# Kernel tuning notes

Measured on AMD Instinct MI355X. Metric: run time of the kernel, lower is better.

The kernel has to match this reference:

```python
import jax, jax.numpy as jnp
import numpy as np

N_FEATURES = 1024
N_HEADS = 16
D_ATTN = 64


def setup_inputs() -> dict:
    key = jax.random.key(0)
    k_x, k_qkv, k_pw, k_pb = jax.random.split(key, 4)
    B, S = 2, 2048
    x = jax.random.normal(k_x, (B, S, N_FEATURES), dtype=jnp.float32)
    # torch nn.Linear weights are [out, in]; init scale ~ 1/sqrt(in)
    w_qkv = jax.random.normal(k_qkv, (3 * N_HEADS * D_ATTN, N_FEATURES), dtype=jnp.float32) / np.sqrt(N_FEATURES)
    w_proj = jax.random.normal(k_pw, (N_FEATURES, N_HEADS * D_ATTN), dtype=jnp.float32) / np.sqrt(N_HEADS * D_ATTN)
    b_proj = jax.random.normal(k_pb, (N_FEATURES,), dtype=jnp.float32) / np.sqrt(N_HEADS * D_ATTN)
    return {"x": x, "w_qkv": w_qkv, "w_proj": w_proj, "b_proj": b_proj}


def reference(x, w_qkv, w_proj, b_proj):
    B, S, F = x.shape
    H, D = N_HEADS, D_ATTN
    # fused QKV projection (bias=False): [B,S,3*H*D]
    qkv = jnp.einsum('bsf,of->bso', x, w_qkv)
    qkv = qkv.reshape(B, S, 3, H, D)
    q = jnp.transpose(qkv[:, :, 0], (0, 2, 1, 3))  # [B,H,S,D]
    k = jnp.transpose(qkv[:, :, 1], (0, 2, 1, 3))
    v = jnp.transpose(qkv[:, :, 2], (0, 2, 1, 3))
    scale = 1.0 / jnp.sqrt(jnp.asarray(D, dtype=x.dtype))
    scores = jnp.einsum('bhqd,bhkd->bhqk', q, k) * scale  # [B,H,S,S]
    attn = jax.nn.softmax(scores, axis=-1)
    out = jnp.einsum('bhqk,bhkd->bhqd', attn, v)  # [B,H,S,D]
    out = jnp.transpose(out, (0, 2, 1, 3)).reshape(B, S, H * D)
    # output projection (dropout is identity in eval mode)
    return jnp.einsum('bsm,fm->bsf', out, w_proj) + b_proj
```

## Files before the change

kernel.cpp:

```cpp
#include <hip/hip_runtime.h>
#include <hip/hip_bf16.h>
#include <math.h>

#define BATCH 2
#define SEQ 2048
#define NFEAT 1024
#define NHEAD 16
#define DHEAD 64
#define MROWS (BATCH * SEQ)
#define NQKV (3 * NHEAD * DHEAD)

typedef __attribute__((ext_vector_type(8))) short short8;
typedef __attribute__((ext_vector_type(4))) float floatx4;

#define CEXP 0.18033688f

__device__ __forceinline__ unsigned short f2bf(float f) {
    unsigned int u = __float_as_uint(f);
    u += 0x7fff + ((u >> 16) & 1);
    return (unsigned short)(u >> 16);
}

__device__ __forceinline__ float fast_exp2(float x) {
    return __builtin_amdgcn_exp2f(x);
}

__device__ __forceinline__ uint pack_bf16x2(float lo, float hi) {
    float2 t; t.x = lo; t.y = hi;
    __hip_bfloat162 h = __float22bfloat162_rn(t);
    union { __hip_bfloat162 h; uint u; } c; c.h = h;
    return c.u;
}

__device__ __forceinline__ void async16(const void* g, void* l) {
    __builtin_amdgcn_global_load_lds(
        (const __attribute__((address_space(1))) void*)g,
        (__attribute__((address_space(3))) void*)l, 16, 0, 0);
}

__global__ void cvt_swz(const float* __restrict__ x, const float* __restrict__ wq,
                        const float* __restrict__ wp,
                        ushort* __restrict__ xb, ushort* __restrict__ wqb,
                        ushort* __restrict__ wpb) {
    const int NX = MROWS * NFEAT / 4, NWQ = NQKV * NFEAT / 4, NWP = NFEAT * NFEAT / 4;
    int i = blockIdx.x * blockDim.x + threadIdx.x;
    if (i >= NX + NWQ + NWP) return;
    const float* src; ushort* dst; int idx4;
    if (i < NX)            { src = x;  dst = xb;  idx4 = i; }
    else if (i < NX + NWQ) { src = wq; dst = wqb; idx4 = i - NX; }
    else                   { src = wp; dst = wpb; idx4 = i - NX - NWQ; }
    float4 v = ((const float4*)src)[idx4];
    ushort4 o;
    o.x = f2bf(v.x); o.y = f2bf(v.y); o.z = f2bf(v.z); o.w = f2bf(v.w);
    const int e = idx4 * 4;
    const int k = e & (NFEAT - 1);
    const int row = e >> 10;
    const int kp = (k & ~31) | (((((k >> 3) & 3) ^ ((row >> 1) & 3))) << 3) | (k & 7);
    *(ushort4*)(dst + (size_t)row * NFEAT + kp) = o;
}

template <int EPI>
__global__ __launch_bounds__(256, 2)
void gemm_bt(const ushort* __restrict__ A, const ushort* __restrict__ W,
             int M, int N, int K,
             ushort* __restrict__ qb, ushort* __restrict__ kb, ushort* __restrict__ vtb,
             const float* __restrict__ bias, float* __restrict__ Cout) {
    __shared__ ushort smem[8192];
    ushort* As = smem;
    ushort* Bs = smem + 4096;
    const int tid = threadIdx.x;
    const int wave = tid >> 6, lane = tid & 63;
    const int m0 = blockIdx.y * 128, n0 = blockIdx.x * 128;
    const int wm = (wave >> 1) * 64, wn = (wave & 1) * 64;
    const int lr = lane & 15, lg = lane >> 4;
    const int kswz = (lg ^ ((lr >> 1) & 3)) * 8;

    floatx4 acc[4][4] = {};

    const int seg0 = tid, seg1 = tid + 256;
    const int row0 = seg0 >> 2, cb0 = (seg0 & 3) * 8;
    const int row1 = seg1 >> 2, cb1 = (seg1 & 3) * 8;

    for (int k0 = 0; k0 < K; k0 += 32) {
        async16(A + (size_t)(m0 + row0) * K + k0 + cb0, (void*)(As + seg0 * 8));
        async16(A + (size_t)(m0 + row1) * K + k0 + cb1, (void*)(As + seg1 * 8));
        async16(W + (size_t)(n0 + row0) * K + k0 + cb0, (void*)(Bs + seg0 * 8));
        async16(W + (size_t)(n0 + row1) * K + k0 + cb1, (void*)(Bs + seg1 * 8));
        __syncthreads();
        short8 a[4], b[4];
#pragma unroll
        for (int i = 0; i < 4; ++i)
            a[i] = *(const short8*)(As + (wm + i * 16 + lr) * 32 + kswz);
#pragma unroll
        for (int j = 0; j < 4; ++j)
            b[j] = *(const short8*)(Bs + (wn + j * 16 + lr) * 32 + kswz);
#pragma unroll
        for (int i = 0; i < 4; ++i)
#pragma unroll
            for (int j = 0; j < 4; ++j)
                acc[i][j] = __builtin_amdgcn_mfma_f32_16x16x32_bf16(a[i], b[j], acc[i][j], 0, 0, 0);
        __syncthreads();
    }

    if (EPI == 1) {
#pragma unroll
        for (int i = 0; i < 4; ++i)
#pragma unroll
            for (int j = 0; j < 4; ++j)
#pragma unroll
                for (int r = 0; r < 4; ++r) {
                    const int m = m0 + wm + i * 16 + lg * 4 + r;
                    const int n = n0 + wn + j * 16 + lr;
                    Cout[(size_t)m * N + n] = acc[i][j][r] + bias[n];
                }
        return;
    }

    const int t = n0 >> 10;
    const int bidx = m0 >> 11;
    if (t < 2) {
#pragma unroll
        for (int i = 0; i < 4; ++i)
#pragma unroll
            for (int j = 0; j < 4; ++j)
#pragma unroll
                for (int r = 0; r < 4; ++r) {
                    const int m = m0 + wm + i * 16 + lg * 4 + r;
                    const int n = n0 + wn + j * 16 + lr;
                    const int s = m & (SEQ - 1);
                    const int rem = n & 1023, h = rem >> 6, d = rem & 63;
                    if (t == 0) {
                        qb[((size_t)(bidx * NHEAD + h) * SEQ + s) * DHEAD + d] =
                            f2bf(acc[i][j][r] * CEXP);
                    } else {
                        const int dcol = ((((d >> 3) ^ (s & 7)) << 3)) | (d & 7);
                        kb[((size_t)(bidx * NHEAD + h) * SEQ + s) * DHEAD + dcol] =
                            f2bf(acc[i][j][r]);
                    }
                }
    } else {
#pragma unroll
        for (int hhalf = 0; hhalf < 2; ++hhalf) {
            if ((wm >> 6) == hhalf) {
#pragma unroll
                for (int i = 0; i < 4; ++i) {
                    const int chunk = i * 2 + (lg >> 1);
#pragma unroll
                    for (int j = 0; j < 4; ++j) {
                        const int n = wn + j * 16 + lr;
                        uint2 pk;
                        pk.x = pack_bf16x2(acc[i][j][0], acc[i][j][1]);
                        pk.y = pack_bf16x2(acc[i][j][2], acc[i][j][3]);
                        *(uint2*)(smem + n * 64 + ((chunk ^ (n & 7)) * 8) + (lg & 1) * 4) = pk;
                    }
                }
            }
            __syncthreads();
            const int s_base = (m0 & (SEQ - 1)) + hhalf * 64;
#pragma unroll
            for (int it = 0; it < 4; ++it) {
                const int n_r = (tid >> 3) + it * 32;
                const int p = tid & 7;
                short8 rowv = *(const short8*)(smem + n_r * 64 + p * 8);
                const int nglob = n0 + n_r;
                const int d = nglob & 63, hh = (nglob & 1023) >> 6;
                *(short8*)(vtb + ((size_t)(bidx * NHEAD + hh) * DHEAD + d) * SEQ + s_base + p * 8) = rowv;
            }
            __syncthreads();
        }
    }
}

__global__ __launch_bounds__(256, 4)
void flash_attn(const ushort* __restrict__ qb, const ushort* __restrict__ kb,
                const ushort* __restrict__ vtb, ushort* __restrict__ aob) {
    const int qt = blockIdx.x, bh = blockIdx.y;
    const int tid = threadIdx.x, wave = tid >> 6, lane = tid & 63;
    const int lr = lane & 15, lg = lane >> 4;

    __shared__ ushort Ks[2][64 * 64];
    __shared__ ushort Vs[2][64 * 64];
    __shared__ ushort Ps_all[4][16 * 64];
    ushort* Ps = Ps_all[wave];

    const ushort* Qb = qb + (size_t)bh * SEQ * DHEAD;
    const ushort* Kb = kb + (size_t)bh * SEQ * DHEAD;
    const ushort* Vt = vtb + (size_t)bh * DHEAD * SEQ;

    const int q0 = qt * 64 + wave * 16;

    short8 qf[2];
#pragma unroll
    for (int kk = 0; kk < 2; ++kk)
        qf[kk] = *(const short8*)(Qb + (size_t)(q0 + lr) * DHEAD + kk * 32 + lg * 8);

    const int kofs = tid * 8;
    const size_t vrow = (size_t)(tid >> 3) * SEQ;
    const int vcol = (tid & 7) * 8;

    async16(Kb + kofs,                    (void*)(Ks[0] + kofs));
    async16(Kb + 2048 + kofs,             (void*)(Ks[0] + 2048 + kofs));
    async16(Vt + vrow + vcol,             (void*)(Vs[0] + kofs));
    async16(Vt + 32 * SEQ + vrow + vcol,  (void*)(Vs[0] + 2048 + kofs));

    floatx4 acc_o[4] = {};
    float l_lane = 0.0f;
    const int sw = lr & 7;

#define FLASH_PREFETCH(BUF, KV)                                                     \
    {                                                                               \
        const int kv_ = (KV);                                                       \
        async16(Kb + (size_t)kv_ * DHEAD + kofs,          (void*)(Ks[BUF] + kofs)); \
        async16(Kb + (size_t)kv_ * DHEAD + 2048 + kofs,   (void*)(Ks[BUF] + 2048 + kofs)); \
        async16(Vt + vrow + kv_ + vcol,                   (void*)(Vs[BUF] + kofs)); \
        async16(Vt + 32 * SEQ + vrow + kv_ + vcol,        (void*)(Vs[BUF] + 2048 + kofs)); \
    }

#define FLASH_COMPUTE(BUF)                                                          \
    {                                                                               \
        floatx4 st[4] = {};                                                         \
        _Pragma("unroll")                                                           \
        for (int kk = 0; kk < 2; ++kk)                                              \
            _Pragma("unroll")                                                       \
            for (int i = 0; i < 4; ++i) {                                           \
                short8 kf = *(const short8*)(Ks[BUF] + (i * 16 + lr) * 64 +         \
                                             (((kk * 4 + lg) ^ sw) * 8));           \
                st[i] = __builtin_amdgcn_mfma_f32_16x16x32_bf16(kf, qf[kk], st[i], 0, 0, 0); \
            }                                                                       \
        _Pragma("unroll")                                                           \
        for (int i = 0; i < 4; ++i) {                                               \
            const float p0 = fast_exp2(st[i][0]);                                   \
            const float p1 = fast_exp2(st[i][1]);                                   \
            const float p2 = fast_exp2(st[i][2]);                                   \
            const float p3 = fast_exp2(st[i][3]);                                   \
            l_lane += (p0 + p1) + (p2 + p3);                                        \
            uint2 pk;                                                               \
            pk.x = pack_bf16x2(p0, p1);                                             \
            pk.y = pack_bf16x2(p2, p3);                                             \
            const int chunk = i * 2 + (lg >> 1);                                    \
            *(uint2*)(Ps + lr * 64 + ((chunk ^ sw) * 8) + (lg & 1) * 4) = pk;       \
        }                                                                           \
        _Pragma("unroll")                                                           \
        for (int kk2 = 0; kk2 < 2; ++kk2) {                                         \
            short8 pf = *(const short8*)(Ps + lr * 64 + (((kk2 * 4 + lg) ^ sw) * 8)); \
            _Pragma("unroll")                                                       \
            for (int j2 = 0; j2 < 4; ++j2) {                                        \
                short8 vf = *(const short8*)(Vs[BUF] + (j2 * 16 + lr) * 64 +        \
                                             (((kk2 * 4 + lg) ^ sw) * 8));          \
                acc_o[j2] = __builtin_amdgcn_mfma_f32_16x16x32_bf16(pf, vf, acc_o[j2], 0, 0, 0); \
            }                                                                       \
        }                                                                           \
    }

    for (int kt = 0; kt < SEQ / 64; kt += 2) {
        __syncthreads();
        FLASH_PREFETCH(1, (kt + 1) * 64)
        FLASH_COMPUTE(0)
        __syncthreads();
        if (kt + 2 < SEQ / 64)
            FLASH_PREFETCH(0, (kt + 2) * 64)
        FLASH_COMPUTE(1)
    }
#undef FLASH_PREFETCH
#undef FLASH_COMPUTE

    l_lane += __shfl_xor(l_lane, 16);
    l_lane += __shfl_xor(l_lane, 32);

    const int b = bh >> 4, h = bh & 15;
#pragma unroll
    for (int r = 0; r < 4; ++r) {
        const float lq = __shfl(l_lane, lg * 4 + r);
        const float invl = 1.0f / lq;
        const int srow = b * SEQ + q0 + lg * 4 + r;
        const int key = (srow >> 1) & 3;
#pragma unroll
        for (int j2 = 0; j2 < 4; ++j2) {
            const int d = j2 * 16 + lr;
            const int dsw = (d & ~31) | (((((d >> 3) & 3) ^ key)) << 3) | (d & 7);
            aob[(size_t)srow * (NHEAD * DHEAD) + h * DHEAD + dsw] = f2bf(acc_o[j2][r] * invl);
        }
    }
}

extern "C" void kernel_launch(void* const* d_in, const int* in_sizes, int n_in,
                              void* d_out, int out_size, void* d_ws, size_t ws_size,
                              hipStream_t stream) {
    const float* x      = (const float*)d_in[0];
    const float* w_qkv  = (const float*)d_in[1];
    const float* w_proj = (const float*)d_in[2];
    const float* b_proj = (const float*)d_in[3];
    float* out = (float*)d_out;

    ushort* ws = (ushort*)d_ws;
    ushort* xb     = ws;
    ushort* wqkvb  = xb + (size_t)MROWS * NFEAT;
    ushort* wprojb = wqkvb + (size_t)NQKV * NFEAT;
    ushort* qb     = wprojb + (size_t)NFEAT * NFEAT;
    ushort* kb     = qb + (size_t)MROWS * NFEAT;
    ushort* vtb    = kb + (size_t)MROWS * NFEAT;
    ushort* aob    = vtb + (size_t)MROWS * NFEAT;

    {
        const int total = (MROWS * NFEAT + NQKV * NFEAT + NFEAT * NFEAT) / 4;
        cvt_swz<<<(total + 255) / 256, 256, 0, stream>>>(x, w_qkv, w_proj, xb, wqkvb, wprojb);
    }

    {
        dim3 grid(NQKV / 128, MROWS / 128);
        gemm_bt<0><<<grid, 256, 0, stream>>>(xb, wqkvb, MROWS, NQKV, NFEAT,
                                             qb, kb, vtb, nullptr, nullptr);
    }

    {
        dim3 grid(SEQ / 64, BATCH * NHEAD);
        flash_attn<<<grid, 256, 0, stream>>>(qb, kb, vtb, aob);
    }

    {
        dim3 grid(NFEAT / 128, MROWS / 128);
        gemm_bt<1><<<grid, 256, 0, stream>>>(aob, wprojb, MROWS, NFEAT, NFEAT,
                                             nullptr, nullptr, nullptr, b_proj, out);
    }
}
```

Before: 194.2 us.

## Process 32 query rows per wave in flash attention and narrow projection GEMM tiles

Flash attention now gives each wave two 16-row query tiles (128 queries per block), so every K and V fragment read from shared memory feeds twice as many MFMAs. This halves the K/V global traffic per query and amortizes the per-tile shared-memory loads. The cost is more registers and doubled P scratch in LDS, so occupancy is lowered to 2 blocks per CU. The output projection moves to a dedicated kernel with 128x64 tiles, doubling its grid from 256 to 512 blocks to fill more CUs.

```diff
diff --git a/kernel.cpp b/kernel.cpp
--- a/kernel.cpp
+++ b/kernel.cpp
@@ -59,12 +59,9 @@
     *(ushort4*)(dst + (size_t)row * NFEAT + kp) = o;
 }
 
-template <int EPI>
 __global__ __launch_bounds__(256, 2)
-void gemm_bt(const ushort* __restrict__ A, const ushort* __restrict__ W,
-             int M, int N, int K,
-             ushort* __restrict__ qb, ushort* __restrict__ kb, ushort* __restrict__ vtb,
-             const float* __restrict__ bias, float* __restrict__ Cout) {
+void gemm_qkv(const ushort* __restrict__ A, const ushort* __restrict__ W,
+              ushort* __restrict__ qb, ushort* __restrict__ kb, ushort* __restrict__ vtb) {
     __shared__ ushort smem[8192];
     ushort* As = smem;
     ushort* Bs = smem + 4096;
@@ -81,11 +78,11 @@
     const int row0 = seg0 >> 2, cb0 = (seg0 & 3) * 8;
     const int row1 = seg1 >> 2, cb1 = (seg1 & 3) * 8;
 
-    for (int k0 = 0; k0 < K; k0 += 32) {
-        async16(A + (size_t)(m0 + row0) * K + k0 + cb0, (void*)(As + seg0 * 8));
-        async16(A + (size_t)(m0 + row1) * K + k0 + cb1, (void*)(As + seg1 * 8));
-        async16(W + (size_t)(n0 + row0) * K + k0 + cb0, (void*)(Bs + seg0 * 8));
-        async16(W + (size_t)(n0 + row1) * K + k0 + cb1, (void*)(Bs + seg1 * 8));
+    for (int k0 = 0; k0 < NFEAT; k0 += 32) {
+        async16(A + (size_t)(m0 + row0) * NFEAT + k0 + cb0, (void*)(As + seg0 * 8));
+        async16(A + (size_t)(m0 + row1) * NFEAT + k0 + cb1, (void*)(As + seg1 * 8));
+        async16(W + (size_t)(n0 + row0) * NFEAT + k0 + cb0, (void*)(Bs + seg0 * 8));
+        async16(W + (size_t)(n0 + row1) * NFEAT + k0 + cb1, (void*)(Bs + seg1 * 8));
         __syncthreads();
         short8 a[4], b[4];
 #pragma unroll
@@ -100,20 +97,6 @@
             for (int j = 0; j < 4; ++j)
                 acc[i][j] = __builtin_amdgcn_mfma_f32_16x16x32_bf16(a[i], b[j], acc[i][j], 0, 0, 0);
         __syncthreads();
-    }
-
-    if (EPI == 1) {
-#pragma unroll
-        for (int i = 0; i < 4; ++i)
-#pragma unroll
-            for (int j = 0; j < 4; ++j)
-#pragma unroll
-                for (int r = 0; r < 4; ++r) {
-                    const int m = m0 + wm + i * 16 + lg * 4 + r;
-                    const int n = n0 + wn + j * 16 + lr;
-                    Cout[(size_t)m * N + n] = acc[i][j][r] + bias[n];
-                }
-        return;
     }
 
     const int t = n0 >> 10;
@@ -171,7 +154,55 @@
     }
 }
 
-__global__ __launch_bounds__(256, 4)
+__global__ __launch_bounds__(256, 2)
+void gemm_proj(const ushort* __restrict__ A, const ushort* __restrict__ W,
+               const float* __restrict__ bias, float* __restrict__ Cout) {
+    __shared__ ushort As[128 * 32];
+    __shared__ ushort Bs[64 * 32];
+    const int tid = threadIdx.x;
+    const int wave = tid >> 6, lane = tid & 63;
+    const int m0 = blockIdx.y * 128, n0 = blockIdx.x * 64;
+    const int wm = (wave >> 1) * 64, wn = (wave & 1) * 32;
+    const int lr = lane & 15, lg = lane >> 4;
+    const int kswz = (lg ^ ((lr >> 1) & 3)) * 8;
+
+    floatx4 acc[4][2] = {};
+
+    const int rowA = tid >> 2, cb = (tid & 3) * 8;
+
+    for (int k0 = 0; k0 < NFEAT; k0 += 32) {
+        async16(A + (size_t)(m0 + rowA) * NFEAT + k0 + cb, (void*)(As + tid * 8));
+        async16(A + (size_t)(m0 + rowA + 64) * NFEAT + k0 + cb, (void*)(As + (tid + 256) * 8));
+        async16(W + (size_t)(n0 + rowA) * NFEAT + k0 + cb, (void*)(Bs + tid * 8));
+        __syncthreads();
+        short8 a[4], b[2];
+#pragma unroll
+        for (int i = 0; i < 4; ++i)
+            a[i] = *(const short8*)(As + (wm + i * 16 + lr) * 32 + kswz);
+#pragma unroll
+        for (int j = 0; j < 2; ++j)
+            b[j] = *(const short8*)(Bs + (wn + j * 16 + lr) * 32 + kswz);
+#pragma unroll
+        for (int i = 0; i < 4; ++i)
+#pragma unroll
+            for (int j = 0; j < 2; ++j)
+                acc[i][j] = __builtin_amdgcn_mfma_f32_16x16x32_bf16(a[i], b[j], acc[i][j], 0, 0, 0);
+        __syncthreads();
+    }
+
+#pragma unroll
+    for (int i = 0; i < 4; ++i)
+#pragma unroll
+        for (int j = 0; j < 2; ++j)
+#pragma unroll
+            for (int r = 0; r < 4; ++r) {
+                const int m = m0 + wm + i * 16 + lg * 4 + r;
+                const int n = n0 + wn + j * 16 + lr;
+                Cout[(size_t)m * NFEAT + n] = acc[i][j][r] + bias[n];
+            }
+}
+
+__global__ __launch_bounds__(256, 2)
 void flash_attn(const ushort* __restrict__ qb, const ushort* __restrict__ kb,
                 const ushort* __restrict__ vtb, ushort* __restrict__ aob) {
     const int qt = blockIdx.x, bh = blockIdx.y;
@@ -180,19 +211,21 @@
 
     __shared__ ushort Ks[2][64 * 64];
     __shared__ ushort Vs[2][64 * 64];
-    __shared__ ushort Ps_all[4][16 * 64];
+    __shared__ ushort Ps_all[4][32 * 64];
     ushort* Ps = Ps_all[wave];
 
     const ushort* Qb = qb + (size_t)bh * SEQ * DHEAD;
     const ushort* Kb = kb + (size_t)bh * SEQ * DHEAD;
     const ushort* Vt = vtb + (size_t)bh * DHEAD * SEQ;
 
-    const int q0 = qt * 64 + wave * 16;
-
-    short8 qf[2];
-#pragma unroll
-    for (int kk = 0; kk < 2; ++kk)
-        qf[kk] = *(const short8*)(Qb + (size_t)(q0 + lr) * DHEAD + kk * 32 + lg * 8);
+    const int q0 = qt * 128 + wave * 32;
+
+    short8 qf[2][2];
+#pragma unroll
+    for (int j = 0; j < 2; ++j)
+#pragma unroll
+        for (int kk = 0; kk < 2; ++kk)
+            qf[j][kk] = *(const short8*)(Qb + (size_t)(q0 + j * 16 + lr) * DHEAD + kk * 32 + lg * 8);
 
     const int kofs = tid * 8;
     const size_t vrow = (size_t)(tid >> 3) * SEQ;
@@ -203,8 +236,8 @@
     async16(Vt + vrow + vcol,             (void*)(Vs[0] + kofs));
     async16(Vt + 32 * SEQ + vrow + vcol,  (void*)(Vs[0] + 2048 + kofs));
 
-    floatx4 acc_o[4] = {};
-    float l_lane = 0.0f;
+    floatx4 acc_o[2][4] = {};
+    float l_lane[2] = {0.0f, 0.0f};
     const int sw = lr & 7;
 
 #define FLASH_PREFETCH(BUF, KV)                                                     \
@@ -218,36 +251,46 @@
 
 #define FLASH_COMPUTE(BUF)                                                          \
     {                                                                               \
-        floatx4 st[4] = {};                                                         \
+        floatx4 st[4][2] = {};                                                      \
         _Pragma("unroll")                                                           \
         for (int kk = 0; kk < 2; ++kk)                                              \
             _Pragma("unroll")                                                       \
             for (int i = 0; i < 4; ++i) {                                           \
                 short8 kf = *(const short8*)(Ks[BUF] + (i * 16 + lr) * 64 +         \
                                              (((kk * 4 + lg) ^ sw) * 8));           \
-                st[i] = __builtin_amdgcn_mfma_f32_16x16x32_bf16(kf, qf[kk], st[i], 0, 0, 0); \
+                _Pragma("unroll")                                                   \
+                for (int j = 0; j < 2; ++j)                                         \
+                    st[i][j] = __builtin_amdgcn_mfma_f32_16x16x32_bf16(kf, qf[j][kk], st[i][j], 0, 0, 0); \
             }                                                                       \
         _Pragma("unroll")                                                           \
-        for (int i = 0; i < 4; ++i) {                                               \
-            const float p0 = fast_exp2(st[i][0]);                                   \
-            const float p1 = fast_exp2(st[i][1]);                                   \
-            const float p2 = fast_exp2(st[i][2]);                                   \
-            const float p3 = fast_exp2(st[i][3]);                                   \
-            l_lane += (p0 + p1) + (p2 + p3);                                        \
-            uint2 pk;                                                               \
-            pk.x = pack_bf16x2(p0, p1);                                             \
-            pk.y = pack_bf16x2(p2, p3);                                             \
-            const int chunk = i * 2 + (lg >> 1);                                    \
-            *(uint2*)(Ps + lr * 64 + ((chunk ^ sw) * 8) + (lg & 1) * 4) = pk;       \
-        }                                                                           \
+        for (int i = 0; i < 4; ++i)                                                 \
+            _Pragma("unroll")                                                       \
+            for (int j = 0; j < 2; ++j) {                                           \
+                const float p0 = fast_exp2(st[i][j][0]);                            \
+                const float p1 = fast_exp2(st[i][j][1]);                            \
+                const float p2 = fast_exp2(st[i][j][2]);                            \
+                const float p3 = fast_exp2(st[i][j][3]);                            \
+                l_lane[j] += (p0 + p1) + (p2 + p3);                                 \
+                uint2 pk;                                                           \
+                pk.x = pack_bf16x2(p0, p1);                                         \
+                pk.y = pack_bf16x2(p2, p3);                                         \
+                const int chunk = i * 2 + (lg >> 1);                                \
+                *(uint2*)(Ps + (j * 16 + lr) * 64 + ((chunk ^ sw) * 8) + (lg & 1) * 4) = pk; \
+            }                                                                       \
         _Pragma("unroll")                                                           \
         for (int kk2 = 0; kk2 < 2; ++kk2) {                                         \
-            short8 pf = *(const short8*)(Ps + lr * 64 + (((kk2 * 4 + lg) ^ sw) * 8)); \
+            short8 vf[4];                                                           \
             _Pragma("unroll")                                                       \
-            for (int j2 = 0; j2 < 4; ++j2) {                                        \
-                short8 vf = *(const short8*)(Vs[BUF] + (j2 * 16 + lr) * 64 +        \
+            for (int j2 = 0; j2 < 4; ++j2)                                          \
+                vf[j2] = *(const short8*)(Vs[BUF] + (j2 * 16 + lr) * 64 +           \
+                                          (((kk2 * 4 + lg) ^ sw) * 8));             \
+            _Pragma("unroll")                                                       \
+            for (int i2 = 0; i2 < 2; ++i2) {                                        \
+                short8 pf = *(const short8*)(Ps + (i2 * 16 + lr) * 64 +             \
                                              (((kk2 * 4 + lg) ^ sw) * 8));          \
-                acc_o[j2] = __builtin_amdgcn_mfma_f32_16x16x32_bf16(pf, vf, acc_o[j2], 0, 0, 0); \
+                _Pragma("unroll")                                                   \
+                for (int j2 = 0; j2 < 4; ++j2)                                      \
+                    acc_o[i2][j2] = __builtin_amdgcn_mfma_f32_16x16x32_bf16(pf, vf[j2], acc_o[i2][j2], 0, 0, 0); \
             }                                                                       \
         }                                                                           \
     }
@@ -264,21 +307,27 @@
 #undef FLASH_PREFETCH
 #undef FLASH_COMPUTE
 
-    l_lane += __shfl_xor(l_lane, 16);
-    l_lane += __shfl_xor(l_lane, 32);
+#pragma unroll
+    for (int j = 0; j < 2; ++j) {
+        l_lane[j] += __shfl_xor(l_lane[j], 16);
+        l_lane[j] += __shfl_xor(l_lane[j], 32);
+    }
 
     const int b = bh >> 4, h = bh & 15;
 #pragma unroll
-    for (int r = 0; r < 4; ++r) {
-        const float lq = __shfl(l_lane, lg * 4 + r);
-        const float invl = 1.0f / lq;
-        const int srow = b * SEQ + q0 + lg * 4 + r;
-        const int key = (srow >> 1) & 3;
-#pragma unroll
-        for (int j2 = 0; j2 < 4; ++j2) {
-            const int d = j2 * 16 + lr;
-            const int dsw = (d & ~31) | (((((d >> 3) & 3) ^ key)) << 3) | (d & 7);
-            aob[(size_t)srow * (NHEAD * DHEAD) + h * DHEAD + dsw] = f2bf(acc_o[j2][r] * invl);
+    for (int i2 = 0; i2 < 2; ++i2) {
+#pragma unroll
+        for (int r = 0; r < 4; ++r) {
+            const float lq = __shfl(l_lane[i2], lg * 4 + r);
+            const float invl = 1.0f / lq;
+            const int srow = b * SEQ + q0 + i2 * 16 + lg * 4 + r;
+            const int key = (srow >> 1) & 3;
+#pragma unroll
+            for (int j2 = 0; j2 < 4; ++j2) {
+                const int d = j2 * 16 + lr;
+                const int dsw = (d & ~31) | (((((d >> 3) & 3) ^ key)) << 3) | (d & 7);
+                aob[(size_t)srow * (NHEAD * DHEAD) + h * DHEAD + dsw] = f2bf(acc_o[i2][j2][r] * invl);
+            }
         }
     }
 }
@@ -308,18 +357,16 @@
 
     {
         dim3 grid(NQKV / 128, MROWS / 128);
-        gemm_bt<0><<<grid, 256, 0, stream>>>(xb, wqkvb, MROWS, NQKV, NFEAT,
-                                             qb, kb, vtb, nullptr, nullptr);
+        gemm_qkv<<<grid, 256, 0, stream>>>(xb, wqkvb, qb, kb, vtb);
     }
 
     {
-        dim3 grid(SEQ / 64, BATCH * NHEAD);
+        dim3 grid(SEQ / 128, BATCH * NHEAD);
         flash_attn<<<grid, 256, 0, stream>>>(qb, kb, vtb, aob);
     }
 
     {
-        dim3 grid(NFEAT / 128, MROWS / 128);
-        gemm_bt<1><<<grid, 256, 0, stream>>>(aob, wprojb, MROWS, NFEAT, NFEAT,
-                                             nullptr, nullptr, nullptr, b_proj, out);
-    }
-}
+        dim3 grid(NFEAT / 64, MROWS / 128);
+        gemm_proj<<<grid, 256, 0, stream>>>(aob, wprojb, b_proj, out);
+    }
+}
```

Measured after the change: 187.9 us. 3.3% less time.
